# Performance work log

Measured on AMD Instinct MI355X. Metric: run time of the kernel, lower is better.

## Reference

```python
import jax, jax.numpy as jnp
import numpy as np

N_HEAD, D_K, D_V, D_MODEL, D_O = 8, 64, 64, 512, 512
B, S = 2, 4096

def setup_inputs() -> dict:
    key = jax.random.key(0)
    ks = jax.random.split(key, 11)
    s = 1.0 / np.sqrt(D_MODEL)
    so = 1.0 / np.sqrt(N_HEAD * D_V)
    return {
        'q': jax.random.normal(ks[0], (B, S, D_MODEL), jnp.float32),
        'k': jax.random.normal(ks[1], (B, S, D_MODEL), jnp.float32),
        'v': jax.random.normal(ks[2], (B, S, D_MODEL), jnp.float32),
        'Wq': jax.random.uniform(ks[3], (D_MODEL, N_HEAD * D_K), jnp.float32, -s, s),
        'bq': jax.random.uniform(ks[4], (N_HEAD * D_K,), jnp.float32, -s, s),
        'Wk': jax.random.uniform(ks[5], (D_MODEL, N_HEAD * D_K), jnp.float32, -s, s),
        'bk': jax.random.uniform(ks[6], (N_HEAD * D_K,), jnp.float32, -s, s),
        'Wv': jax.random.uniform(ks[7], (D_MODEL, N_HEAD * D_V), jnp.float32, -s, s),
        'bv': jax.random.uniform(ks[8], (N_HEAD * D_V,), jnp.float32, -s, s),
        'Wo': jax.random.uniform(ks[9], (N_HEAD * D_V, D_O), jnp.float32, -so, so),
        'bo': jax.random.uniform(ks[10], (D_O,), jnp.float32, -so, so),
    }

def reference(q, k, v, Wq, bq, Wk, bk, Wv, bv, Wo, bo):
    b, nq, _ = q.shape
    nk = k.shape[1]
    scale = jnp.asarray(np.power(D_K, 0.5), q.dtype)
    # project and split heads: [b, s, h, d]
    qh = (q @ Wq + bq).reshape(b, nq, N_HEAD, D_K)
    kh = (k @ Wk + bk).reshape(b, nk, N_HEAD, D_K)
    vh = (v @ Wv + bv).reshape(b, nk, N_HEAD, D_V)
    # scaled dot-product attention (full score matrix, as in original)
    scores = jnp.einsum('bqhd,bkhd->bhqk', qh, kh) / scale
    attn = jax.nn.softmax(scores, axis=-1)
    out = jnp.einsum('bhqk,bkhd->bqhd', attn, vh)
    # concat heads (head-major over d_v, matching the original view) and output proj
    out = out.reshape(b, nq, N_HEAD * D_V)
    return out @ Wo + bo
```

## Files before the change

### kernel.cpp

```cpp
#include <hip/hip_runtime.h>
#include <hip/hip_bf16.h>

#define NHEAD 8
#define DK_ 64
#define DM_ 512
#define S_LEN 4096
#define NTOK 8192

typedef __bf16 bf16x8 __attribute__((ext_vector_type(8)));
typedef float f32x4 __attribute__((ext_vector_type(4)));

__device__ __forceinline__ unsigned short f2bf(float f) {
    union { float f; unsigned u; } x; x.f = f;
    unsigned u = x.u;
    u += 0x7FFFu + ((u >> 16) & 1u);
    return (unsigned short)(u >> 16);
}

#define GLOAD_LDS16(gptr, ldsbase) \
    __builtin_amdgcn_global_load_lds((const __attribute__((address_space(1))) unsigned int*)(gptr), \
                                     (__attribute__((address_space(3))) unsigned int*)(ldsbase), 16, 0, 0)

__global__ __launch_bounds__(256) void wtrans(const float* __restrict__ Wq, const float* __restrict__ Wk,
                                              const float* __restrict__ Wv, const float* __restrict__ Wo,
                                              unsigned short* __restrict__ Wt) {
    int z = blockIdx.z;
    const float* W = (z == 0) ? Wq : (z == 1) ? Wk : (z == 2) ? Wv : Wo;
    unsigned short* out = Wt + (size_t)z * DM_ * DM_;
    __shared__ float t[64][65];
    int bn = blockIdx.x * 64, bk = blockIdx.y * 64;
    int tid = threadIdx.x;
    int r0 = tid >> 4, c4 = (tid & 15) * 4;
#pragma unroll
    for (int i = 0; i < 4; i++) {
        int r = r0 + i * 16;
        float4 v = *(const float4*)&W[(size_t)(bk + r) * DM_ + bn + c4];
        t[r][c4] = v.x; t[r][c4 + 1] = v.y; t[r][c4 + 2] = v.z; t[r][c4 + 3] = v.w;
    }
    __syncthreads();
    int n0 = tid >> 4, k4 = (tid & 15) * 4;
#pragma unroll
    for (int i = 0; i < 4; i++) {
        int n = n0 + i * 16;
        ushort4 o;
        o.x = f2bf(t[k4 + 0][n]); o.y = f2bf(t[k4 + 1][n]);
        o.z = f2bf(t[k4 + 2][n]); o.w = f2bf(t[k4 + 3][n]);
        *(ushort4*)&out[(size_t)(bn + n) * DM_ + bk + k4] = o;
    }
}

__global__ __launch_bounds__(256, 3) void qkv_proj(const float* __restrict__ xq, const float* __restrict__ xk,
                                                   const float* __restrict__ xv, const unsigned short* __restrict__ Wt,
                                                   const float* __restrict__ bq, const float* __restrict__ bk,
                                                   const float* __restrict__ bv,
                                                   unsigned short* __restrict__ Qh, unsigned short* __restrict__ Kh,
                                                   unsigned short* __restrict__ VhT) {
    int z = blockIdx.z;
    const float* X = (z == 0) ? xq : (z == 1) ? xk : xv;
    const unsigned short* W = Wt + (size_t)z * DM_ * DM_;
    const float* bias = (z == 0) ? bq : (z == 1) ? bk : bv;
    unsigned short* out = (z == 0) ? Qh : (z == 1) ? Kh : VhT;
    float scale = (z == 0) ? 0.125f : 1.0f;

    __shared__ unsigned short As[128 * 40];
    __shared__ unsigned short Bs[128 * 40];
    int tid = threadIdx.x;
    int n0 = blockIdx.x * 128, m0 = blockIdx.y * 128;
    int w = tid >> 6, lane = tid & 63;
    int ln = lane & 15, qd = lane >> 4;
    int mb = (w >> 1) * 64, nb = (w & 1) * 64;

    f32x4 acc[4][4];
#pragma unroll
    for (int i = 0; i < 4; i++)
#pragma unroll
        for (int j = 0; j < 4; j++) { f32x4 zz = {0.f, 0.f, 0.f, 0.f}; acc[i][j] = zz; }

    for (int kk = 0; kk < DM_; kk += 32) {
        __syncthreads();
#pragma unroll
        for (int i = 0; i < 4; i++) {
            int idx = i * 256 + tid;
            int row = idx >> 3, k4 = (idx & 7) * 4;
            float4 v = *(const float4*)&X[(size_t)(m0 + row) * DM_ + kk + k4];
            ushort4 o; o.x = f2bf(v.x); o.y = f2bf(v.y); o.z = f2bf(v.z); o.w = f2bf(v.w);
            *(ushort4*)&As[row * 40 + k4] = o;
        }
#pragma unroll
        for (int i = 0; i < 2; i++) {
            int idx = i * 256 + tid;
            int row = idx >> 2, k8 = (idx & 3) * 8;
            uint4 v = *(const uint4*)&W[(size_t)(n0 + row) * DM_ + kk + k8];
            *(uint4*)&Bs[row * 40 + k8] = v;
        }
        __syncthreads();
        bf16x8 af[4], bf[4];
#pragma unroll
        for (int mt = 0; mt < 4; mt++) af[mt] = *(const bf16x8*)&As[(mb + mt * 16 + ln) * 40 + qd * 8];
#pragma unroll
        for (int nt = 0; nt < 4; nt++) bf[nt] = *(const bf16x8*)&Bs[(nb + nt * 16 + ln) * 40 + qd * 8];
#pragma unroll
        for (int mt = 0; mt < 4; mt++)
#pragma unroll
            for (int nt = 0; nt < 4; nt++)
                acc[mt][nt] = __builtin_amdgcn_mfma_f32_16x16x32_bf16(af[mt], bf[nt], acc[mt][nt], 0, 0, 0);
    }

    float bvv[4];
#pragma unroll
    for (int nt = 0; nt < 4; nt++) bvv[nt] = bias[n0 + nb + nt * 16 + ln];
#pragma unroll
    for (int mt = 0; mt < 4; mt++) {
        int mrow0 = m0 + mb + mt * 16 + qd * 4;
        int b = mrow0 >> 12, s = mrow0 & 4095;
#pragma unroll
        for (int nt = 0; nt < 4; nt++) {
            int ncol = n0 + nb + nt * 16 + ln;
            int h = ncol >> 6, d = ncol & 63;
            if (z == 2) {
                ushort4 o;
                o.x = f2bf((acc[mt][nt][0] + bvv[nt]) * scale);
                o.y = f2bf((acc[mt][nt][1] + bvv[nt]) * scale);
                o.z = f2bf((acc[mt][nt][2] + bvv[nt]) * scale);
                o.w = f2bf((acc[mt][nt][3] + bvv[nt]) * scale);
                *(ushort4*)&out[((size_t)(b * NHEAD + h) * DK_ + d) * S_LEN + s] = o;
            } else {
#pragma unroll
                for (int r = 0; r < 4; r++)
                    out[((size_t)(b * NHEAD + h) * S_LEN + (s + r)) * DK_ + d] =
                        f2bf((acc[mt][nt][r] + bvv[nt]) * scale);
            }
        }
    }
}

__global__ __launch_bounds__(256, 2) void flash_attn(const unsigned short* __restrict__ Qh,
                                                     const unsigned short* __restrict__ Kh,
                                                     const unsigned short* __restrict__ VhT,
                                                     unsigned short* __restrict__ Ao) {
    __shared__ unsigned short Ks[64 * 64];
    __shared__ unsigned short Vs[64 * 64];
    __shared__ unsigned short Pl[4 * 32 * 72];
    int i = blockIdx.x;
    int bh = (i & 7) + 8 * ((i >> 3) & 1);
    int qb = i >> 4;
    int tid = threadIdx.x;
    int w = tid >> 6, lane = tid & 63;
    int ln = lane & 15, qd = lane >> 4;
    int sw = ln & 7;
    int q0 = qb * 128 + w * 32;
    const unsigned short* Qp = Qh + (size_t)bh * S_LEN * DK_;
    const unsigned short* Kp = Kh + (size_t)bh * S_LEN * DK_;
    const unsigned short* Vp = VhT + (size_t)bh * DK_ * S_LEN;
    unsigned short* pb = &Pl[w * 32 * 72];

    int sr = lane >> 3;
    int sc = (lane & 7) ^ sr;
    const unsigned short* ksrc = Kp + (size_t)(w * 16 + sr) * DK_ + sc * 8;
    const unsigned short* vsrc = Vp + (size_t)(w * 16 + sr) * S_LEN + sc * 8;
    unsigned short* kdst0 = &Ks[w * 1024];
    unsigned short* kdst1 = &Ks[w * 1024 + 512];
    unsigned short* vdst0 = &Vs[w * 1024];
    unsigned short* vdst1 = &Vs[w * 1024 + 512];

    bf16x8 qfA0 = *(const bf16x8*)&Qp[(size_t)(q0 + ln) * DK_ + qd * 8];
    bf16x8 qfA1 = *(const bf16x8*)&Qp[(size_t)(q0 + ln) * DK_ + qd * 8 + 32];
    bf16x8 qfB0 = *(const bf16x8*)&Qp[(size_t)(q0 + 16 + ln) * DK_ + qd * 8];
    bf16x8 qfB1 = *(const bf16x8*)&Qp[(size_t)(q0 + 16 + ln) * DK_ + qd * 8 + 32];

    f32x4 oacc[2][4];
#pragma unroll
    for (int f = 0; f < 2; f++)
#pragma unroll
        for (int j = 0; j < 4; j++) { f32x4 z = {0.f, 0.f, 0.f, 0.f}; oacc[f][j] = z; }
    f32x4 lsum[2];
    { f32x4 z = {0.f, 0.f, 0.f, 0.f}; lsum[0] = z; lsum[1] = z; }

    for (int ks = 0; ks < S_LEN; ks += 64) {
        __syncthreads();

        GLOAD_LDS16(ksrc + (size_t)ks * DK_, kdst0);
        GLOAD_LDS16(ksrc + (size_t)(ks + 8) * DK_, kdst1);
        GLOAD_LDS16(vsrc + ks, vdst0);
        GLOAD_LDS16(vsrc + (size_t)8 * S_LEN + ks, vdst1);

        __syncthreads();

        f32x4 stA[4], stB[4];
#pragma unroll
        for (int t = 0; t < 4; t++) {
            bf16x8 kf0 = *(const bf16x8*)&Ks[(t * 16 + ln) * 64 + (qd ^ sw) * 8];
            bf16x8 kf1 = *(const bf16x8*)&Ks[(t * 16 + ln) * 64 + ((qd + 4) ^ sw) * 8];
            f32x4 zA = {0.f, 0.f, 0.f, 0.f}, zB = {0.f, 0.f, 0.f, 0.f};
            zA = __builtin_amdgcn_mfma_f32_16x16x32_bf16(kf0, qfA0, zA, 0, 0, 0);
            zA = __builtin_amdgcn_mfma_f32_16x16x32_bf16(kf1, qfA1, zA, 0, 0, 0);
            zB = __builtin_amdgcn_mfma_f32_16x16x32_bf16(kf0, qfB0, zB, 0, 0, 0);
            zB = __builtin_amdgcn_mfma_f32_16x16x32_bf16(kf1, qfB1, zB, 0, 0, 0);
            stA[t] = zA; stB[t] = zB;
        }
#pragma unroll
        for (int t = 0; t < 4; t++) {
            f32x4 eA, eB;
#pragma unroll
            for (int r = 0; r < 4; r++) { eA[r] = __expf(stA[t][r]); eB[r] = __expf(stB[t][r]); }
            lsum[0] += eA; lsum[1] += eB;
            ushort4 oA, oB;
            oA.x = f2bf(eA[0]); oA.y = f2bf(eA[1]); oA.z = f2bf(eA[2]); oA.w = f2bf(eA[3]);
            oB.x = f2bf(eB[0]); oB.y = f2bf(eB[1]); oB.z = f2bf(eB[2]); oB.w = f2bf(eB[3]);
            *(ushort4*)&pb[(ln) * 72 + t * 16 + qd * 4] = oA;
            *(ushort4*)&pb[(16 + ln) * 72 + t * 16 + qd * 4] = oB;
        }
        bf16x8 pA0 = *(const bf16x8*)&pb[ln * 72 + qd * 8];
        bf16x8 pA1 = *(const bf16x8*)&pb[ln * 72 + 32 + qd * 8];
        bf16x8 pB0 = *(const bf16x8*)&pb[(16 + ln) * 72 + qd * 8];
        bf16x8 pB1 = *(const bf16x8*)&pb[(16 + ln) * 72 + 32 + qd * 8];
#pragma unroll
        for (int dt = 0; dt < 4; dt++) {
            bf16x8 vf0 = *(const bf16x8*)&Vs[(dt * 16 + ln) * 64 + (qd ^ sw) * 8];
            bf16x8 vf1 = *(const bf16x8*)&Vs[(dt * 16 + ln) * 64 + ((qd + 4) ^ sw) * 8];
            oacc[0][dt] = __builtin_amdgcn_mfma_f32_16x16x32_bf16(vf0, pA0, oacc[0][dt], 0, 0, 0);
            oacc[0][dt] = __builtin_amdgcn_mfma_f32_16x16x32_bf16(vf1, pA1, oacc[0][dt], 0, 0, 0);
            oacc[1][dt] = __builtin_amdgcn_mfma_f32_16x16x32_bf16(vf0, pB0, oacc[1][dt], 0, 0, 0);
            oacc[1][dt] = __builtin_amdgcn_mfma_f32_16x16x32_bf16(vf1, pB1, oacc[1][dt], 0, 0, 0);
        }
    }

    int bb = bh >> 3, hh = bh & 7;
#pragma unroll
    for (int f = 0; f < 2; f++) {
        float l = lsum[f][0] + lsum[f][1] + lsum[f][2] + lsum[f][3];
        l += __shfl_xor(l, 16, 64);
        l += __shfl_xor(l, 32, 64);
        float inv = 1.0f / l;
        int token = bb * S_LEN + q0 + f * 16 + ln;
#pragma unroll
        for (int dt = 0; dt < 4; dt++) {
            ushort4 o;
            o.x = f2bf(oacc[f][dt][0] * inv);
            o.y = f2bf(oacc[f][dt][1] * inv);
            o.z = f2bf(oacc[f][dt][2] * inv);
            o.w = f2bf(oacc[f][dt][3] * inv);
            *(ushort4*)&Ao[(size_t)token * DM_ + hh * DK_ + dt * 16 + qd * 4] = o;
        }
    }
}

__global__ __launch_bounds__(256) void out_gemm(const unsigned short* __restrict__ A,
                                                const unsigned short* __restrict__ Wt,
                                                const float* __restrict__ bias, float* __restrict__ out) {
    __shared__ unsigned short As[128 * 40];
    __shared__ unsigned short Bs[128 * 40];
    int tid = threadIdx.x;
    int n0 = blockIdx.x * 128, m0 = blockIdx.y * 128;
    int w = tid >> 6, lane = tid & 63;
    int ln = lane & 15, qd = lane >> 4;
    int mb = (w >> 1) * 64, nb = (w & 1) * 64;

    f32x4 acc[4][4];
#pragma unroll
    for (int i = 0; i < 4; i++)
#pragma unroll
        for (int j = 0; j < 4; j++) { f32x4 z = {0.f, 0.f, 0.f, 0.f}; acc[i][j] = z; }

    for (int kk = 0; kk < DM_; kk += 32) {
        __syncthreads();
#pragma unroll
        for (int i = 0; i < 2; i++) {
            int idx = i * 256 + tid;
            int row = idx >> 2, k8 = (idx & 3) * 8;
            uint4 va = *(const uint4*)&A[(size_t)(m0 + row) * DM_ + kk + k8];
            *(uint4*)&As[row * 40 + k8] = va;
            uint4 vb = *(const uint4*)&Wt[(size_t)(n0 + row) * DM_ + kk + k8];
            *(uint4*)&Bs[row * 40 + k8] = vb;
        }
        __syncthreads();
        bf16x8 af[4], bf[4];
#pragma unroll
        for (int mt = 0; mt < 4; mt++) af[mt] = *(const bf16x8*)&As[(mb + mt * 16 + ln) * 40 + qd * 8];
#pragma unroll
        for (int nt = 0; nt < 4; nt++) bf[nt] = *(const bf16x8*)&Bs[(nb + nt * 16 + ln) * 40 + qd * 8];
#pragma unroll
        for (int mt = 0; mt < 4; mt++)
#pragma unroll
            for (int nt = 0; nt < 4; nt++)
                acc[mt][nt] = __builtin_amdgcn_mfma_f32_16x16x32_bf16(af[mt], bf[nt], acc[mt][nt], 0, 0, 0);
    }

    float bv[4];
#pragma unroll
    for (int nt = 0; nt < 4; nt++) bv[nt] = bias[n0 + nb + nt * 16 + ln];
#pragma unroll
    for (int mt = 0; mt < 4; mt++) {
        int mrow0 = m0 + mb + mt * 16 + qd * 4;
#pragma unroll
        for (int nt = 0; nt < 4; nt++) {
            int ncol = n0 + nb + nt * 16 + ln;
#pragma unroll
            for (int r = 0; r < 4; r++)
                out[(size_t)(mrow0 + r) * DM_ + ncol] = acc[mt][nt][r] + bv[nt];
        }
    }
}

extern "C" void kernel_launch(void* const* d_in, const int* in_sizes, int n_in,
                              void* d_out, int out_size, void* d_ws, size_t ws_size,
                              hipStream_t stream) {
    const float* q  = (const float*)d_in[0];
    const float* k  = (const float*)d_in[1];
    const float* v  = (const float*)d_in[2];
    const float* Wq = (const float*)d_in[3];
    const float* bq = (const float*)d_in[4];
    const float* Wk = (const float*)d_in[5];
    const float* bk = (const float*)d_in[6];
    const float* Wv = (const float*)d_in[7];
    const float* bv = (const float*)d_in[8];
    const float* Wo = (const float*)d_in[9];
    const float* bo = (const float*)d_in[10];
    float* out = (float*)d_out;

    unsigned short* Wt  = (unsigned short*)d_ws;
    unsigned short* Qh  = Wt + (size_t)4 * DM_ * DM_;
    unsigned short* Kh  = Qh + (size_t)NTOK * DM_;
    unsigned short* VhT = Kh + (size_t)NTOK * DM_;
    unsigned short* Ao  = VhT + (size_t)NTOK * DM_;

    wtrans<<<dim3(8, 8, 4), 256, 0, stream>>>(Wq, Wk, Wv, Wo, Wt);
    qkv_proj<<<dim3(4, 64, 3), 256, 0, stream>>>(q, k, v, Wt, bq, bk, bv, Qh, Kh, VhT);
    flash_attn<<<dim3(512), 256, 0, stream>>>(Qh, Kh, VhT, Ao);
    out_gemm<<<dim3(4, 64), 256, 0, stream>>>(Ao, Wt + (size_t)3 * DM_ * DM_, bo, out);
}
```

Measured before the change: 248.2 us.

## Double-buffer K/V tiles, use exp2 with folded log2e, MFMA row sums, packed bf16

The attention loop now double-buffers the K and V tiles in LDS, issuing the async global-to-LDS loads for the next tile before computing on the current one. This drops one barrier per iteration and overlaps memory traffic with MFMA work. The log2(e) factor is folded into the Q scale so the softmax can use a hardware exp2. Row sums are computed with an MFMA against a ones vector, replacing the VALU accumulation and cross-lane shuffles, and float-to-bf16 conversions use the packed hardware convert where available. The ones-MFMA sums bf16-rounded P values, which differs slightly from the fp32 sum. Double-buffering also doubles K/V LDS use, which could affect occupancy.

```diff
diff --git a/kernel.cpp b/kernel.cpp
--- a/kernel.cpp
+++ b/kernel.cpp
@@ -16,6 +16,23 @@
     u += 0x7FFFu + ((u >> 16) & 1u);
     return (unsigned short)(u >> 16);
 }
+
+#if __has_builtin(__builtin_amdgcn_cvt_pk_bf16_f32)
+__device__ __forceinline__ unsigned int pkbf(float a, float b) {
+    auto r = __builtin_amdgcn_cvt_pk_bf16_f32(a, b);
+    unsigned int u; __builtin_memcpy(&u, &r, 4); return u;
+}
+#else
+__device__ __forceinline__ unsigned int pkbf(float a, float b) {
+    return (unsigned)f2bf(a) | ((unsigned)f2bf(b) << 16);
+}
+#endif
+
+#if __has_builtin(__builtin_amdgcn_exp2f)
+#define EXP2F(x) __builtin_amdgcn_exp2f(x)
+#else
+#define EXP2F(x) exp2f(x)
+#endif
 
 #define GLOAD_LDS16(gptr, ldsbase) \
     __builtin_amdgcn_global_load_lds((const __attribute__((address_space(1))) unsigned int*)(gptr), \
@@ -60,7 +77,7 @@
     const unsigned short* W = Wt + (size_t)z * DM_ * DM_;
     const float* bias = (z == 0) ? bq : (z == 1) ? bk : bv;
     unsigned short* out = (z == 0) ? Qh : (z == 1) ? Kh : VhT;
-    float scale = (z == 0) ? 0.125f : 1.0f;
+    float scale = (z == 0) ? 0.125f * 1.44269504f : 1.0f;
 
     __shared__ unsigned short As[128 * 40];
     __shared__ unsigned short Bs[128 * 40];
@@ -83,8 +100,8 @@
             int idx = i * 256 + tid;
             int row = idx >> 3, k4 = (idx & 7) * 4;
             float4 v = *(const float4*)&X[(size_t)(m0 + row) * DM_ + kk + k4];
-            ushort4 o; o.x = f2bf(v.x); o.y = f2bf(v.y); o.z = f2bf(v.z); o.w = f2bf(v.w);
-            *(ushort4*)&As[row * 40 + k4] = o;
+            uint2 o; o.x = pkbf(v.x, v.y); o.y = pkbf(v.z, v.w);
+            *(uint2*)&As[row * 40 + k4] = o;
         }
 #pragma unroll
         for (int i = 0; i < 2; i++) {
@@ -118,12 +135,10 @@
             int ncol = n0 + nb + nt * 16 + ln;
             int h = ncol >> 6, d = ncol & 63;
             if (z == 2) {
-                ushort4 o;
-                o.x = f2bf((acc[mt][nt][0] + bvv[nt]) * scale);
-                o.y = f2bf((acc[mt][nt][1] + bvv[nt]) * scale);
-                o.z = f2bf((acc[mt][nt][2] + bvv[nt]) * scale);
-                o.w = f2bf((acc[mt][nt][3] + bvv[nt]) * scale);
-                *(ushort4*)&out[((size_t)(b * NHEAD + h) * DK_ + d) * S_LEN + s] = o;
+                uint2 o;
+                o.x = pkbf((acc[mt][nt][0] + bvv[nt]) * scale, (acc[mt][nt][1] + bvv[nt]) * scale);
+                o.y = pkbf((acc[mt][nt][2] + bvv[nt]) * scale, (acc[mt][nt][3] + bvv[nt]) * scale);
+                *(uint2*)&out[((size_t)(b * NHEAD + h) * DK_ + d) * S_LEN + s] = o;
             } else {
 #pragma unroll
                 for (int r = 0; r < 4; r++)
@@ -138,8 +153,8 @@
                                                      const unsigned short* __restrict__ Kh,
                                                      const unsigned short* __restrict__ VhT,
                                                      unsigned short* __restrict__ Ao) {
-    __shared__ unsigned short Ks[64 * 64];
-    __shared__ unsigned short Vs[64 * 64];
+    __shared__ unsigned short Ks[2][64 * 64];
+    __shared__ unsigned short Vs[2][64 * 64];
     __shared__ unsigned short Pl[4 * 32 * 72];
     int i = blockIdx.x;
     int bh = (i & 7) + 8 * ((i >> 3) & 1);
@@ -158,39 +173,48 @@
     int sc = (lane & 7) ^ sr;
     const unsigned short* ksrc = Kp + (size_t)(w * 16 + sr) * DK_ + sc * 8;
     const unsigned short* vsrc = Vp + (size_t)(w * 16 + sr) * S_LEN + sc * 8;
-    unsigned short* kdst0 = &Ks[w * 1024];
-    unsigned short* kdst1 = &Ks[w * 1024 + 512];
-    unsigned short* vdst0 = &Vs[w * 1024];
-    unsigned short* vdst1 = &Vs[w * 1024 + 512];
 
     bf16x8 qfA0 = *(const bf16x8*)&Qp[(size_t)(q0 + ln) * DK_ + qd * 8];
     bf16x8 qfA1 = *(const bf16x8*)&Qp[(size_t)(q0 + ln) * DK_ + qd * 8 + 32];
     bf16x8 qfB0 = *(const bf16x8*)&Qp[(size_t)(q0 + 16 + ln) * DK_ + qd * 8];
     bf16x8 qfB1 = *(const bf16x8*)&Qp[(size_t)(q0 + 16 + ln) * DK_ + qd * 8 + 32];
 
+    bf16x8 ones;
+#pragma unroll
+    for (int j = 0; j < 8; j++) ones[j] = (__bf16)1.0f;
+
     f32x4 oacc[2][4];
 #pragma unroll
     for (int f = 0; f < 2; f++)
 #pragma unroll
         for (int j = 0; j < 4; j++) { f32x4 z = {0.f, 0.f, 0.f, 0.f}; oacc[f][j] = z; }
-    f32x4 lsum[2];
-    { f32x4 z = {0.f, 0.f, 0.f, 0.f}; lsum[0] = z; lsum[1] = z; }
-
-    for (int ks = 0; ks < S_LEN; ks += 64) {
-        __syncthreads();
-
-        GLOAD_LDS16(ksrc + (size_t)ks * DK_, kdst0);
-        GLOAD_LDS16(ksrc + (size_t)(ks + 8) * DK_, kdst1);
-        GLOAD_LDS16(vsrc + ks, vdst0);
-        GLOAD_LDS16(vsrc + (size_t)8 * S_LEN + ks, vdst1);
-
-        __syncthreads();
+    f32x4 lacc[2];
+    { f32x4 z = {0.f, 0.f, 0.f, 0.f}; lacc[0] = z; lacc[1] = z; }
+
+    GLOAD_LDS16(ksrc, &Ks[0][w * 1024]);
+    GLOAD_LDS16(ksrc + (size_t)8 * DK_, &Ks[0][w * 1024 + 512]);
+    GLOAD_LDS16(vsrc, &Vs[0][w * 1024]);
+    GLOAD_LDS16(vsrc + (size_t)8 * S_LEN, &Vs[0][w * 1024 + 512]);
+
+    int p = 0;
+    for (int ks = 0; ks < S_LEN; ks += 64, p ^= 1) {
+        __syncthreads();
+        if (ks + 64 < S_LEN) {
+            const unsigned short* kn = ksrc + (size_t)(ks + 64) * DK_;
+            const unsigned short* vn = vsrc + (ks + 64);
+            GLOAD_LDS16(kn, &Ks[p ^ 1][w * 1024]);
+            GLOAD_LDS16(kn + (size_t)8 * DK_, &Ks[p ^ 1][w * 1024 + 512]);
+            GLOAD_LDS16(vn, &Vs[p ^ 1][w * 1024]);
+            GLOAD_LDS16(vn + (size_t)8 * S_LEN, &Vs[p ^ 1][w * 1024 + 512]);
+        }
+        const unsigned short* KsT = &Ks[p][0];
+        const unsigned short* VsT = &Vs[p][0];
 
         f32x4 stA[4], stB[4];
 #pragma unroll
         for (int t = 0; t < 4; t++) {
-            bf16x8 kf0 = *(const bf16x8*)&Ks[(t * 16 + ln) * 64 + (qd ^ sw) * 8];
-            bf16x8 kf1 = *(const bf16x8*)&Ks[(t * 16 + ln) * 64 + ((qd + 4) ^ sw) * 8];
+            bf16x8 kf0 = *(const bf16x8*)&KsT[(t * 16 + ln) * 64 + (qd ^ sw) * 8];
+            bf16x8 kf1 = *(const bf16x8*)&KsT[(t * 16 + ln) * 64 + ((qd + 4) ^ sw) * 8];
             f32x4 zA = {0.f, 0.f, 0.f, 0.f}, zB = {0.f, 0.f, 0.f, 0.f};
             zA = __builtin_amdgcn_mfma_f32_16x16x32_bf16(kf0, qfA0, zA, 0, 0, 0);
             zA = __builtin_amdgcn_mfma_f32_16x16x32_bf16(kf1, qfA1, zA, 0, 0, 0);
@@ -200,24 +224,27 @@
         }
 #pragma unroll
         for (int t = 0; t < 4; t++) {
-            f32x4 eA, eB;
-#pragma unroll
-            for (int r = 0; r < 4; r++) { eA[r] = __expf(stA[t][r]); eB[r] = __expf(stB[t][r]); }
-            lsum[0] += eA; lsum[1] += eB;
-            ushort4 oA, oB;
-            oA.x = f2bf(eA[0]); oA.y = f2bf(eA[1]); oA.z = f2bf(eA[2]); oA.w = f2bf(eA[3]);
-            oB.x = f2bf(eB[0]); oB.y = f2bf(eB[1]); oB.z = f2bf(eB[2]); oB.w = f2bf(eB[3]);
-            *(ushort4*)&pb[(ln) * 72 + t * 16 + qd * 4] = oA;
-            *(ushort4*)&pb[(16 + ln) * 72 + t * 16 + qd * 4] = oB;
-        }
+            uint2 a, b;
+            a.x = pkbf(EXP2F(stA[t][0]), EXP2F(stA[t][1]));
+            a.y = pkbf(EXP2F(stA[t][2]), EXP2F(stA[t][3]));
+            b.x = pkbf(EXP2F(stB[t][0]), EXP2F(stB[t][1]));
+            b.y = pkbf(EXP2F(stB[t][2]), EXP2F(stB[t][3]));
+            *(uint2*)&pb[ln * 72 + t * 16 + qd * 4] = a;
+            *(uint2*)&pb[(16 + ln) * 72 + t * 16 + qd * 4] = b;
+        }
+        asm volatile("" ::: "memory");
         bf16x8 pA0 = *(const bf16x8*)&pb[ln * 72 + qd * 8];
         bf16x8 pA1 = *(const bf16x8*)&pb[ln * 72 + 32 + qd * 8];
         bf16x8 pB0 = *(const bf16x8*)&pb[(16 + ln) * 72 + qd * 8];
         bf16x8 pB1 = *(const bf16x8*)&pb[(16 + ln) * 72 + 32 + qd * 8];
+        lacc[0] = __builtin_amdgcn_mfma_f32_16x16x32_bf16(ones, pA0, lacc[0], 0, 0, 0);
+        lacc[0] = __builtin_amdgcn_mfma_f32_16x16x32_bf16(ones, pA1, lacc[0], 0, 0, 0);
+        lacc[1] = __builtin_amdgcn_mfma_f32_16x16x32_bf16(ones, pB0, lacc[1], 0, 0, 0);
+        lacc[1] = __builtin_amdgcn_mfma_f32_16x16x32_bf16(ones, pB1, lacc[1], 0, 0, 0);
 #pragma unroll
         for (int dt = 0; dt < 4; dt++) {
-            bf16x8 vf0 = *(const bf16x8*)&Vs[(dt * 16 + ln) * 64 + (qd ^ sw) * 8];
-            bf16x8 vf1 = *(const bf16x8*)&Vs[(dt * 16 + ln) * 64 + ((qd + 4) ^ sw) * 8];
+            bf16x8 vf0 = *(const bf16x8*)&VsT[(dt * 16 + ln) * 64 + (qd ^ sw) * 8];
+            bf16x8 vf1 = *(const bf16x8*)&VsT[(dt * 16 + ln) * 64 + ((qd + 4) ^ sw) * 8];
             oacc[0][dt] = __builtin_amdgcn_mfma_f32_16x16x32_bf16(vf0, pA0, oacc[0][dt], 0, 0, 0);
             oacc[0][dt] = __builtin_amdgcn_mfma_f32_16x16x32_bf16(vf1, pA1, oacc[0][dt], 0, 0, 0);
             oacc[1][dt] = __builtin_amdgcn_mfma_f32_16x16x32_bf16(vf0, pB0, oacc[1][dt], 0, 0, 0);
@@ -228,19 +255,14 @@
     int bb = bh >> 3, hh = bh & 7;
 #pragma unroll
     for (int f = 0; f < 2; f++) {
-        float l = lsum[f][0] + lsum[f][1] + lsum[f][2] + lsum[f][3];
-        l += __shfl_xor(l, 16, 64);
-        l += __shfl_xor(l, 32, 64);
-        float inv = 1.0f / l;
+        float inv = 1.0f / lacc[f][0];
         int token = bb * S_LEN + q0 + f * 16 + ln;
 #pragma unroll
         for (int dt = 0; dt < 4; dt++) {
-            ushort4 o;
-            o.x = f2bf(oacc[f][dt][0] * inv);
-            o.y = f2bf(oacc[f][dt][1] * inv);
-            o.z = f2bf(oacc[f][dt][2] * inv);
-            o.w = f2bf(oacc[f][dt][3] * inv);
-            *(ushort4*)&Ao[(size_t)token * DM_ + hh * DK_ + dt * 16 + qd * 4] = o;
+            uint2 o;
+            o.x = pkbf(oacc[f][dt][0] * inv, oacc[f][dt][1] * inv);
+            o.y = pkbf(oacc[f][dt][2] * inv, oacc[f][dt][3] * inv);
+            *(uint2*)&Ao[(size_t)token * DM_ + hh * DK_ + dt * 16 + qd * 4] = o;
         }
     }
 }
```

Measured after the change: 251.5 us. Within noise of the previous version (+1.3%).
